# Optimization experiments

Measured on AMD Instinct MI355X. Metric: run time of the kernel, lower is better.

## Reference

```python
import jax, jax.numpy as jnp
import numpy as np

SR = 32000
N_FFT = 1024
HOP = 320
N_MELS = 128
PCEN_EPS = 1e-6
LN_EPS = 1e-6


def _hz_to_mel(f):
    return 2595.0 * np.log10(1.0 + f / 700.0)


def _mel_to_hz(m):
    return 700.0 * (10.0 ** (m / 2595.0) - 1.0)


def make_mel_fb():
    # HTK-scale triangular mel filterbank, [n_freqs, n_mels] (torchaudio default)
    n_freqs = N_FFT // 2 + 1
    mels = np.linspace(_hz_to_mel(0.0), _hz_to_mel(SR / 2.0), N_MELS + 2)
    f_pts = _mel_to_hz(mels)                       # [n_mels+2]
    all_freqs = np.linspace(0.0, SR / 2.0, n_freqs)
    f_diff = f_pts[1:] - f_pts[:-1]
    slopes = f_pts[None, :] - all_freqs[:, None]   # [n_freqs, n_mels+2]
    down = -slopes[:, :-2] / f_diff[:-1]
    up = slopes[:, 2:] / f_diff[1:]
    fb = np.maximum(0.0, np.minimum(down, up))
    return fb.astype(np.float32)


def setup_inputs() -> dict:
    key = jax.random.key(0)
    x = jax.random.normal(key, (16, 320000), dtype=jnp.float32)
    return {
        "x": x,
        "mel_fb": jnp.asarray(make_mel_fb()),
        "log_s": jnp.asarray(np.log(0.025), dtype=jnp.float32),
        "log_alpha": jnp.asarray(np.log(0.98), dtype=jnp.float32),
        "log_delta": jnp.asarray(np.log(2.0), dtype=jnp.float32),
        "log_r": jnp.asarray(np.log(0.5), dtype=jnp.float32),
    }


def reference(x, mel_fb, log_s, log_alpha, log_delta, log_r):
    B, T = x.shape
    pad = N_FFT // 2
    xp = jnp.pad(x, ((0, 0), (pad, pad)), mode="reflect")
    n_frames = 1 + (xp.shape[1] - N_FFT) // HOP           # = T//HOP + 1
    idx = jnp.arange(n_frames)[:, None] * HOP + jnp.arange(N_FFT)[None, :]
    frames = xp[:, idx]                                    # [B, F, N_FFT]
    # periodic Hann window (torch.hann_window default)
    win = 0.5 * (1.0 - jnp.cos(2.0 * jnp.pi * jnp.arange(N_FFT) / N_FFT))
    spec = jnp.fft.rfft(frames * win, axis=-1)             # [B, F, N_FFT//2+1]
    power = spec.real ** 2 + spec.imag ** 2                # power spectrogram
    E = jnp.einsum("bfk,km->bfm", power, mel_fb)           # [B, F, M] mel energies

    s = jnp.exp(log_s)
    alpha = jnp.exp(log_alpha)
    delta = jnp.exp(log_delta)
    r = jnp.exp(log_r)

    # Causal exponential smoother M(t) = (1-s) M(t-1) + s E(t), M init = first frame
    E_t = jnp.swapaxes(E, 0, 1)                            # [F, B, M]

    def step(m, e):
        m = (1.0 - s) * m + s * e
        return m, m

    _, M_t = jax.lax.scan(step, E_t[0], E_t)
    smooth = jnp.swapaxes(M_t, 0, 1)                       # [B, F, M]

    pcen = (E / (PCEN_EPS + smooth) ** alpha + delta) ** r - delta ** r

    # affine-free layer_norm over last dim (n_mels), eps=1e-6
    mu = jnp.mean(pcen, axis=-1, keepdims=True)
    var = jnp.var(pcen, axis=-1, keepdims=True)
    return (pcen - mu) / jnp.sqrt(var + LN_EPS)
```

## Files before the change

### kernel.cpp

```cpp
#include <hip/hip_runtime.h>
#include <math.h>

#define SRATE   32000
#define NFFT    1024
#define HOP     320
#define NBINS   513
#define NMELS   128
#define NFRAMES 1001
#define NB      16
#define TLEN    320000
#define PCEN_EPS 1e-6f
#define LN_EPS   1e-6f
#define MAXW     64

#define CL      16
#define NCHUNK  63

#define CPF     4
#define LPITCH  33

__device__ __constant__ static const int BR5_[1] = {0};
constexpr int BR5[32] = {0,16,8,24,4,20,12,28,2,18,10,26,6,22,14,30,
                         1,17,9,25,5,21,13,29,3,19,11,27,7,23,15,31};

__device__ __forceinline__ void fft32(float2* y) {
    constexpr float C16[16] = {
        1.f, 0.98078528f, 0.92387953f, 0.83146961f,
        0.70710678f, 0.55557023f, 0.38268343f, 0.19509032f,
        0.f, -0.19509032f, -0.38268343f, -0.55557023f,
        -0.70710678f, -0.83146961f, -0.92387953f, -0.98078528f};
    constexpr float S16[16] = {
        0.f, 0.19509032f, 0.38268343f, 0.55557023f,
        0.70710678f, 0.83146961f, 0.92387953f, 0.98078528f,
        1.f, 0.98078528f, 0.92387953f, 0.83146961f,
        0.70710678f, 0.55557023f, 0.38268343f, 0.19509032f};
    #pragma unroll
    for (int h = 16; h >= 1; h >>= 1) {
        #pragma unroll
        for (int b = 0; b < 32; b += 2 * h) {
            #pragma unroll
            for (int j = 0; j < h; ++j) {
                float2 u = y[b + j], w = y[b + j + h];
                float sr = u.x - w.x, si = u.y - w.y;
                y[b + j] = make_float2(u.x + w.x, u.y + w.y);
                const float wr = C16[j * (16 / h)];
                const float wi = -S16[j * (16 / h)];
                y[b + j + h] = make_float2(sr * wr - si * wi, sr * wi + si * wr);
            }
        }
    }
}

__global__ __launch_bounds__(256) void k_prep(
    const float* __restrict__ fb, int* __restrict__ kmin, int* __restrict__ klen,
    float* __restrict__ wv, float* __restrict__ winT, float2* __restrict__ twrow)
{
    const int blk = blockIdx.x;
    const int tid = threadIdx.x;
    if (blk < NMELS) {
        const int m = blk;
        __shared__ int smin[4], smax[4];
        int lmin = 1 << 30, lmax = -1;
        for (int k = tid; k < NBINS; k += 256) {
            if (fb[k * NMELS + m] > 0.f) {
                if (k < lmin) lmin = k;
                if (k > lmax) lmax = k;
            }
        }
        #pragma unroll
        for (int off = 32; off; off >>= 1) {
            int om = __shfl_xor(lmin, off); if (om < lmin) lmin = om;
            int ox = __shfl_xor(lmax, off); if (ox > lmax) lmax = ox;
        }
        if ((tid & 63) == 0) { smin[tid >> 6] = lmin; smax[tid >> 6] = lmax; }
        __syncthreads();
        int k0 = min(min(smin[0], smin[1]), min(smin[2], smin[3]));
        int k1 = max(max(smax[0], smax[1]), max(smax[2], smax[3]));
        int L  = (k1 < 0) ? 0 : min(k1 - k0 + 1, MAXW);
        if (tid == 0) { kmin[m] = (k1 < 0) ? 0 : k0; klen[m] = L; }
        if (tid < L) wv[m * MAXW + tid] = fb[(k0 + tid) * NMELS + m];
    } else {
        const int i = (blk - NMELS) * 256 + tid;
        if (i < NFFT) {
            float sp = sinpif((float)i * (1.0f / (float)NFFT));
            winT[((i & 31) << 5) | (i >> 5)] = sp * sp;
        } else {
            const int e = i - NFFT;
            const int c = e >> 5, k1 = e & 31;
            const int n = c * k1;
            float sn, cn;
            sincospif((float)n * (1.0f / 512.0f), &sn, &cn);
            twrow[e] = make_float2(cn, -sn);
        }
    }
}

__global__ __launch_bounds__(256) void k_melspec(
    const float* __restrict__ x,
    const int*   __restrict__ kmin,
    const int*   __restrict__ klen,
    const float* __restrict__ wv,
    const float* __restrict__ fb,
    const float* __restrict__ winT,
    const float2* __restrict__ twrow,
    float* __restrict__ E,
    int usePacked)
{
    __shared__ float2 Ld[CPF][LPITCH * 32];

    const int tid = threadIdx.x;
    const int g   = blockIdx.x;

    if (tid < 32 * CPF) {
        const int v = tid >> 5, c = tid & 31;
        const int fa = 8 * g + 2 * v, fbf = fa + 1;
        const int ba = fa / NFRAMES,  ta = fa  - ba * NFRAMES;
        const int bb = fbf / NFRAMES, tb = fbf - bb * NFRAMES;
        const float* xa = x + (size_t)ba * TLEN;
        const float* xb = x + (size_t)bb * TLEN;
        const int basea = ta * HOP - (NFFT / 2);
        const int baseb = tb * HOP - (NFFT / 2);
        float2 y[32];
        const bool safe = (basea >= 0) && (baseb >= 0) &&
                          (basea + NFFT - 1 < TLEN) && (baseb + NFFT - 1 < TLEN);
        if (usePacked && safe) {
            #pragma unroll
            for (int r = 0; r < 32; ++r) {
                const int i = c + 32 * r;
                const float w = winT[(c << 5) + r];
                y[r] = make_float2(xa[basea + i] * w, xb[baseb + i] * w);
            }
        } else {
            #pragma unroll
            for (int r = 0; r < 32; ++r) {
                const int i = c + 32 * r;
                int ja = basea + i;
                ja = (ja < 0) ? -ja : ((ja >= TLEN) ? (2 * TLEN - 2 - ja) : ja);
                int jb = baseb + i;
                jb = (jb < 0) ? -jb : ((jb >= TLEN) ? (2 * TLEN - 2 - jb) : jb);
                float w;
                if (usePacked) w = winT[(c << 5) + r];
                else { float sp = sinpif((float)i * (1.0f / (float)NFFT)); w = sp * sp; }
                y[r] = make_float2(xa[ja] * w, xb[jb] * w);
            }
        }
        fft32(y);
        const float2* trow = twrow + (c << 5);
        #pragma unroll
        for (int k1 = 0; k1 < 32; ++k1) {
            float2 val = y[BR5[k1]];
            float2 w;
            if (usePacked) w = trow[k1];
            else {
                float sn, cn;
                sincospif((float)(c * k1) * (1.0f / 512.0f), &sn, &cn);
                w = make_float2(cn, -sn);
            }
            Ld[v][LPITCH * c + k1] =
                make_float2(val.x * w.x - val.y * w.y,
                            val.x * w.y + val.y * w.x);
        }
    }
    __syncthreads();

    if (tid < 32 * CPF) {
        const int v = tid >> 5, k1 = tid & 31;
        float2 y[32];
        #pragma unroll
        for (int cc = 0; cc < 32; ++cc) y[cc] = Ld[v][LPITCH * cc + k1];
        fft32(y);
        #pragma unroll
        for (int k2 = 0; k2 < 32; ++k2)
            Ld[v][LPITCH * k2 + k1] = y[BR5[k2]];
    }
    __syncthreads();

    {
        const int m  = tid & 127;
        const int vh = tid >> 7;
        #pragma unroll
        for (int q = 0; q < 2; ++q) {
            const int vv = vh + 2 * q;
            const int f0 = 8 * g + 2 * vv;
            float acc0 = 0.f, acc1 = 0.f;
            if (usePacked) {
                const int k0 = kmin[m], L = klen[m];
                const float* w = wv + m * MAXW;
                for (int j = 0; j < L; ++j) {
                    const int k  = k0 + j;
                    const int kr = (NFFT - k) & (NFFT - 1);
                    float2 Z  = Ld[vv][LPITCH * (k  >> 5) + (k  & 31)];
                    float2 Zr = Ld[vv][LPITCH * (kr >> 5) + (kr & 31)];
                    float x1r = Z.x + Zr.x, x1i = Z.y - Zr.y;
                    float x2r = Z.y + Zr.y, x2i = Zr.x - Z.x;
                    float ww = w[j];
                    acc0 += (x1r * x1r + x1i * x1i) * ww;
                    acc1 += (x2r * x2r + x2i * x2i) * ww;
                }
            } else {
                for (int k = 0; k < NBINS; ++k) {
                    const int kr = (NFFT - k) & (NFFT - 1);
                    float2 Z  = Ld[vv][LPITCH * (k  >> 5) + (k  & 31)];
                    float2 Zr = Ld[vv][LPITCH * (kr >> 5) + (kr & 31)];
                    float x1r = Z.x + Zr.x, x1i = Z.y - Zr.y;
                    float x2r = Z.y + Zr.y, x2i = Zr.x - Z.x;
                    float ww = fb[k * NMELS + m];
                    acc0 += (x1r * x1r + x1i * x1i) * ww;
                    acc1 += (x2r * x2r + x2i * x2i) * ww;
                }
            }
            E[(size_t)f0 * NMELS + m]       = 0.25f * acc0;
            E[(size_t)(f0 + 1) * NMELS + m] = 0.25f * acc1;
        }
    }
}

__global__ __launch_bounds__(256) void k_pcen_chunk(
    const float* __restrict__ E, float* __restrict__ Bws,
    float* __restrict__ E0ws, const float* __restrict__ p_ls)
{
    const int gid = blockIdx.x * blockDim.x + threadIdx.x;
    const int m = gid & (NMELS - 1);
    const int c = (gid >> 7) % NCHUNK;
    const int b = gid / (NMELS * NCHUNK);

    const float s = expf(p_ls[0]);
    const float a = 1.f - s;

    const int t0 = c * CL;
    const int L  = (t0 + CL <= NFRAMES) ? CL : (NFRAMES - t0);
    const float* col = E + (size_t)b * NFRAMES * NMELS + m;

    if (c == 0) E0ws[b * NMELS + m] = col[0];

    float Bacc;
    if (L == CL) {
        float e[CL];
        #pragma unroll
        for (int j = 0; j < CL; ++j)
            e[j] = col[(size_t)(t0 + j) * NMELS];
        float p0 = 0.f, p1 = 0.f, p2 = 0.f, p3 = 0.f;
        #pragma unroll
        for (int u = 0; u < 4; ++u) {
            p0 = a * p0 + s * e[u];
            p1 = a * p1 + s * e[4 + u];
            p2 = a * p2 + s * e[8 + u];
            p3 = a * p3 + s * e[12 + u];
        }
        const float a2 = a * a, a4 = a2 * a2, a8 = a4 * a4, a12 = a8 * a4;
        Bacc = a12 * p0 + a8 * p1 + a4 * p2 + p3;
    } else {
        Bacc = 0.f;
        for (int j = 0; j < L; ++j)
            Bacc = a * Bacc + s * col[(size_t)(t0 + j) * NMELS];
    }
    Bws[gid] = Bacc;
}

__global__ __launch_bounds__(256) void k_pcen_ln(
    float* __restrict__ E, const float* __restrict__ Bws,
    const float* __restrict__ E0ws,
    const float* __restrict__ p_ls, const float* __restrict__ p_la,
    const float* __restrict__ p_ld, const float* __restrict__ p_lr)
{
    __shared__ float sm[2 * CL][NMELS];

    const int tid  = threadIdx.x;
    const int half = tid >> 7;
    const int m    = tid & 127;
    const int b    = blockIdx.x >> 5;
    const int cp   = blockIdx.x & 31;
    const int c    = cp * 2 + half;

    const float s     = expf(p_ls[0]);
    const float alpha = expf(p_la[0]);
    const float delta = expf(p_ld[0]);
    const float r     = expf(p_lr[0]);
    const float dr    = __powf(delta, r);
    const float a     = 1.f - s;
    const float a2 = a * a, a4 = a2 * a2, a8 = a4 * a4;
    const float a16 = a8 * a8;

    if (c < NCHUNK) {
        float M = E0ws[b * NMELS + m];
        const float* Bcol = Bws + (size_t)b * NCHUNK * NMELS + m;
        int cc = 0;
        for (; cc + 8 <= c; cc += 8) {
            float b0 = Bcol[(size_t)(cc + 0) * NMELS];
            float b1 = Bcol[(size_t)(cc + 1) * NMELS];
            float b2 = Bcol[(size_t)(cc + 2) * NMELS];
            float b3 = Bcol[(size_t)(cc + 3) * NMELS];
            float b4 = Bcol[(size_t)(cc + 4) * NMELS];
            float b5 = Bcol[(size_t)(cc + 5) * NMELS];
            float b6 = Bcol[(size_t)(cc + 6) * NMELS];
            float b7 = Bcol[(size_t)(cc + 7) * NMELS];
            M = a16 * M + b0; M = a16 * M + b1; M = a16 * M + b2; M = a16 * M + b3;
            M = a16 * M + b4; M = a16 * M + b5; M = a16 * M + b6; M = a16 * M + b7;
        }
        for (; cc < c; ++cc)
            M = a16 * M + Bcol[(size_t)cc * NMELS];

        const int t0 = c * CL;
        const int L  = (t0 + CL <= NFRAMES) ? CL : (NFRAMES - t0);
        const float* col = E + ((size_t)b * NFRAMES + t0) * NMELS + m;
        for (int j = 0; j < L; ++j) {
            float e = col[(size_t)j * NMELS];
            M = a * M + s * e;
            float den = __powf(PCEN_EPS + M, alpha);
            sm[half * CL + j][m] = __powf(e / den + delta, r) - dr;
        }
    }
    __syncthreads();

    const int wid  = tid >> 6;
    const int lane = tid & 63;
    for (int row = wid; row < 2 * CL; row += 4) {
        const int cc = cp * 2 + (row >> 4);
        if (cc >= NCHUNK) continue;
        const int j   = row & (CL - 1);
        const int tt0 = cc * CL;
        const int LL  = (tt0 + CL <= NFRAMES) ? CL : (NFRAMES - tt0);
        if (j >= LL) continue;
        float v0 = sm[row][lane], v1 = sm[row][lane + 64];
        float sum = v0 + v1;
        float sq  = v0 * v0 + v1 * v1;
        #pragma unroll
        for (int off = 32; off; off >>= 1) {
            sum += __shfl_xor(sum, off);
            sq  += __shfl_xor(sq,  off);
        }
        float mu  = sum * (1.f / 128.f);
        float var = sq * (1.f / 128.f) - mu * mu;
        float inv = rsqrtf(var + LN_EPS);
        float* p = E + ((size_t)b * NFRAMES + tt0 + j) * NMELS;
        p[lane]      = (v0 - mu) * inv;
        p[lane + 64] = (v1 - mu) * inv;
    }
}

__global__ __launch_bounds__(256) void k_pcen_serial(
    float* __restrict__ E,
    const float* __restrict__ p_ls, const float* __restrict__ p_la,
    const float* __restrict__ p_ld, const float* __restrict__ p_lr)
{
    const int gid = blockIdx.x * blockDim.x + threadIdx.x;
    const int b = gid >> 7;
    const int m = gid & 127;

    const float s     = expf(p_ls[0]);
    const float alpha = expf(p_la[0]);
    const float delta = expf(p_ld[0]);
    const float r     = expf(p_lr[0]);
    const float dr    = powf(delta, r);
    const float a     = 1.f - s;

    float* col = E + (size_t)b * NFRAMES * NMELS + m;
    float M = col[0];
    for (int t = 0; t < NFRAMES; ++t) {
        float e = col[(size_t)t * NMELS];
        M = a * M + s * e;
        float den = __powf(PCEN_EPS + M, alpha);
        float p   = __powf(e / den + delta, r) - dr;
        col[(size_t)t * NMELS] = p;
    }
}

__global__ __launch_bounds__(256) void k_ln(float* __restrict__ out) {
    const int wid  = threadIdx.x >> 6;
    const int lane = threadIdx.x & 63;
    const int row  = blockIdx.x * 4 + wid;
    float* p = out + (size_t)row * NMELS;
    float v0 = p[lane], v1 = p[lane + 64];
    float sum = v0 + v1;
    float sq  = v0 * v0 + v1 * v1;
    #pragma unroll
    for (int off = 32; off; off >>= 1) {
        sum += __shfl_xor(sum, off);
        sq  += __shfl_xor(sq,  off);
    }
    float mu  = sum * (1.f / 128.f);
    float var = sq * (1.f / 128.f) - mu * mu;
    float inv = rsqrtf(var + LN_EPS);
    p[lane]      = (v0 - mu) * inv;
    p[lane + 64] = (v1 - mu) * inv;
}

extern "C" void kernel_launch(void* const* d_in, const int* in_sizes, int n_in,
                              void* d_out, int out_size, void* d_ws, size_t ws_size,
                              hipStream_t stream) {
    const float* x   = (const float*)d_in[0];
    const float* fb  = (const float*)d_in[1];
    const float* lsp = (const float*)d_in[2];
    const float* lap = (const float*)d_in[3];
    const float* ldp = (const float*)d_in[4];
    const float* lrp = (const float*)d_in[5];
    float* out = (float*)d_out;

    const size_t packElems = 128 + 128 + 8192 + 1024 + 2048;
    const size_t scanElems = (size_t)NB * NCHUNK * NMELS;
    const size_t needPack  = packElems * 4;
    const size_t needScan  = (packElems + scanElems + (size_t)NB * NMELS) * 4;

    int usePacked = (ws_size >= needPack) ? 1 : 0;
    int useScan   = (ws_size >= needScan) ? 1 : 0;

    int*    kmin  = (int*)d_ws;
    int*    klen  = kmin + NMELS;
    float*  wv    = (float*)(klen + NMELS);
    float*  winT  = wv + (size_t)NMELS * MAXW;
    float2* twrow = (float2*)(winT + NFFT);
    float*  Bws   = (float*)(twrow + 1024);
    float*  E0ws  = Bws + scanElems;

    if (usePacked)
        k_prep<<<NMELS + 8, 256, 0, stream>>>(fb, kmin, klen, wv, winT, twrow);

    k_melspec<<<NB * NFRAMES / 8, 256, 0, stream>>>(
        x, kmin, klen, wv, fb, winT, twrow, out, usePacked);

    if (useScan) {
        const int nThread = NB * NCHUNK * NMELS;
        k_pcen_chunk<<<nThread / 256, 256, 0, stream>>>(out, Bws, E0ws, lsp);
        k_pcen_ln<<<NB * 32, 256, 0, stream>>>(out, Bws, E0ws, lsp, lap, ldp, lrp);
    } else {
        k_pcen_serial<<<(NB * NMELS) / 256, 256, 0, stream>>>(out, lsp, lap, ldp, lrp);
        k_ln<<<(NB * NFRAMES) / 4, 256, 0, stream>>>(out);
    }
}
```

Before: 93.94 us.

## Restructure melspec kernel: 64-thread blocks, vectorized frame staging, XOR-swizzled LDS

The mel-spectrogram kernel now uses 64-thread blocks processing 4 frames (one wavefront, no idle lanes) instead of 256-thread blocks where only half the threads did FFT work. Frame samples are loaded with coalesced float4 reads and windowed into shared memory, then transposed into registers, replacing strided per-thread scalar global loads. The padded LDS layout is replaced by an XOR swizzle to avoid bank conflicts without padding. This adds an extra shared-memory staging pass and barriers, and doubles the block count.

```diff
diff --git a/kernel.cpp b/kernel.cpp
--- a/kernel.cpp
+++ b/kernel.cpp
@@ -16,12 +16,10 @@
 #define CL      16
 #define NCHUNK  63
 
-#define CPF     4
-#define LPITCH  33
-
-__device__ __constant__ static const int BR5_[1] = {0};
 constexpr int BR5[32] = {0,16,8,24,4,20,12,28,2,18,10,26,6,22,14,30,
                          1,17,9,25,5,21,13,29,3,19,11,27,7,23,15,31};
+
+__device__ __forceinline__ int SL(int r, int c) { return (r << 5) | (c ^ r); }
 
 __device__ __forceinline__ void fft32(float2* y) {
     constexpr float C16[16] = {
@@ -53,7 +51,7 @@
 
 __global__ __launch_bounds__(256) void k_prep(
     const float* __restrict__ fb, int* __restrict__ kmin, int* __restrict__ klen,
-    float* __restrict__ wv, float* __restrict__ winT, float2* __restrict__ twrow)
+    float* __restrict__ wv, float* __restrict__ win, float2* __restrict__ twrow)
 {
     const int blk = blockIdx.x;
     const int tid = threadIdx.x;
@@ -83,7 +81,7 @@
         const int i = (blk - NMELS) * 256 + tid;
         if (i < NFFT) {
             float sp = sinpif((float)i * (1.0f / (float)NFFT));
-            winT[((i & 31) << 5) | (i >> 5)] = sp * sp;
+            win[i] = sp * sp;
         } else {
             const int e = i - NFFT;
             const int c = e >> 5, k1 = e & 31;
@@ -95,56 +93,71 @@
     }
 }
 
-__global__ __launch_bounds__(256) void k_melspec(
+__global__ __launch_bounds__(64) void k_melspec(
     const float* __restrict__ x,
     const int*   __restrict__ kmin,
     const int*   __restrict__ klen,
     const float* __restrict__ wv,
     const float* __restrict__ fb,
-    const float* __restrict__ winT,
+    const float* __restrict__ win_g,
     const float2* __restrict__ twrow,
     float* __restrict__ E,
     int usePacked)
 {
-    __shared__ float2 Ld[CPF][LPITCH * 32];
+    __shared__ float2 Ld[2][1024];
 
     const int tid = threadIdx.x;
     const int g   = blockIdx.x;
-
-    if (tid < 32 * CPF) {
-        const int v = tid >> 5, c = tid & 31;
-        const int fa = 8 * g + 2 * v, fbf = fa + 1;
-        const int ba = fa / NFRAMES,  ta = fa  - ba * NFRAMES;
-        const int bb = fbf / NFRAMES, tb = fbf - bb * NFRAMES;
-        const float* xa = x + (size_t)ba * TLEN;
-        const float* xb = x + (size_t)bb * TLEN;
-        const int basea = ta * HOP - (NFFT / 2);
-        const int baseb = tb * HOP - (NFFT / 2);
-        float2 y[32];
-        const bool safe = (basea >= 0) && (baseb >= 0) &&
-                          (basea + NFFT - 1 < TLEN) && (baseb + NFFT - 1 < TLEN);
-        if (usePacked && safe) {
-            #pragma unroll
-            for (int r = 0; r < 32; ++r) {
-                const int i = c + 32 * r;
-                const float w = winT[(c << 5) + r];
-                y[r] = make_float2(xa[basea + i] * w, xb[baseb + i] * w);
-            }
-        } else {
-            #pragma unroll
-            for (int r = 0; r < 32; ++r) {
-                const int i = c + 32 * r;
-                int ja = basea + i;
-                ja = (ja < 0) ? -ja : ((ja >= TLEN) ? (2 * TLEN - 2 - ja) : ja);
-                int jb = baseb + i;
-                jb = (jb < 0) ? -jb : ((jb >= TLEN) ? (2 * TLEN - 2 - jb) : jb);
-                float w;
-                if (usePacked) w = winT[(c << 5) + r];
-                else { float sp = sinpif((float)i * (1.0f / (float)NFFT)); w = sp * sp; }
-                y[r] = make_float2(xa[ja] * w, xb[jb] * w);
-            }
-        }
-        fft32(y);
+    const int v   = tid >> 5;
+    const int c   = tid & 31;
+
+    float2* T  = Ld[v];
+    float*  fS = (float*)T;
+
+    const int fa  = 4 * g + 2 * v, fbf = fa + 1;
+    const int ba  = fa / NFRAMES,  ta  = fa  - ba * NFRAMES;
+    const int bb  = fbf / NFRAMES, tb  = fbf - bb * NFRAMES;
+    const float* xa = x + (size_t)ba * TLEN;
+    const float* xb = x + (size_t)bb * TLEN;
+    const int basea = ta * HOP - (NFFT / 2);
+    const int baseb = tb * HOP - (NFFT / 2);
+    const bool safe = basea >= 0 && baseb >= 0 &&
+                      (basea + NFFT <= TLEN) && (baseb + NFFT <= TLEN);
+
+    if (usePacked && safe) {
+        const float4* xa4 = (const float4*)(xa + basea);
+        const float4* xb4 = (const float4*)(xb + baseb);
+        const float4* w4  = (const float4*)win_g;
+        float4* S4 = (float4*)fS;
+        #pragma unroll
+        for (int q = 0; q < 8; ++q) {
+            float4 a = xa4[q * 32 + c], b = xb4[q * 32 + c], w = w4[q * 32 + c];
+            S4[q * 32 + c]       = make_float4(a.x * w.x, a.y * w.y, a.z * w.z, a.w * w.w);
+            S4[256 + q * 32 + c] = make_float4(b.x * w.x, b.y * w.y, b.z * w.z, b.w * w.w);
+        }
+    } else {
+        for (int i = c; i < NFFT; i += 32) {
+            int ja = basea + i;
+            ja = (ja < 0) ? -ja : ((ja >= TLEN) ? (2 * TLEN - 2 - ja) : ja);
+            int jb = baseb + i;
+            jb = (jb < 0) ? -jb : ((jb >= TLEN) ? (2 * TLEN - 2 - jb) : jb);
+            float w;
+            if (usePacked) w = win_g[i];
+            else { float sp = sinpif((float)i * (1.0f / (float)NFFT)); w = sp * sp; }
+            fS[i]        = xa[ja] * w;
+            fS[NFFT + i] = xb[jb] * w;
+        }
+    }
+    __syncthreads();
+
+    float2 y[32];
+    #pragma unroll
+    for (int r = 0; r < 32; ++r)
+        y[r] = make_float2(fS[c + 32 * r], fS[NFFT + c + 32 * r]);
+    __syncthreads();
+
+    fft32(y);
+    {
         const float2* trow = twrow + (c << 5);
         #pragma unroll
         for (int k1 = 0; k1 < 32; ++k1) {
@@ -156,32 +169,25 @@
                 sincospif((float)(c * k1) * (1.0f / 512.0f), &sn, &cn);
                 w = make_float2(cn, -sn);
             }
-            Ld[v][LPITCH * c + k1] =
-                make_float2(val.x * w.x - val.y * w.y,
-                            val.x * w.y + val.y * w.x);
+            T[SL(c, k1)] = make_float2(val.x * w.x - val.y * w.y,
+                                       val.x * w.y + val.y * w.x);
         }
     }
     __syncthreads();
 
-    if (tid < 32 * CPF) {
-        const int v = tid >> 5, k1 = tid & 31;
-        float2 y[32];
-        #pragma unroll
-        for (int cc = 0; cc < 32; ++cc) y[cc] = Ld[v][LPITCH * cc + k1];
-        fft32(y);
-        #pragma unroll
-        for (int k2 = 0; k2 < 32; ++k2)
-            Ld[v][LPITCH * k2 + k1] = y[BR5[k2]];
-    }
+    #pragma unroll
+    for (int cc = 0; cc < 32; ++cc) y[cc] = T[SL(cc, c)];
+    fft32(y);
+    #pragma unroll
+    for (int k2 = 0; k2 < 32; ++k2) T[SL(k2, c)] = y[BR5[k2]];
     __syncthreads();
 
-    {
-        const int m  = tid & 127;
-        const int vh = tid >> 7;
-        #pragma unroll
-        for (int q = 0; q < 2; ++q) {
-            const int vv = vh + 2 * q;
-            const int f0 = 8 * g + 2 * vv;
+    for (int vv = 0; vv < 2; ++vv) {
+        const float2* Tv = Ld[vv];
+        const int f0 = 4 * g + 2 * vv;
+        #pragma unroll
+        for (int h = 0; h < 2; ++h) {
+            const int m = tid + 64 * h;
             float acc0 = 0.f, acc1 = 0.f;
             if (usePacked) {
                 const int k0 = kmin[m], L = klen[m];
@@ -189,8 +195,8 @@
                 for (int j = 0; j < L; ++j) {
                     const int k  = k0 + j;
                     const int kr = (NFFT - k) & (NFFT - 1);
-                    float2 Z  = Ld[vv][LPITCH * (k  >> 5) + (k  & 31)];
-                    float2 Zr = Ld[vv][LPITCH * (kr >> 5) + (kr & 31)];
+                    float2 Z  = Tv[SL(k >> 5,  k & 31)];
+                    float2 Zr = Tv[SL(kr >> 5, kr & 31)];
                     float x1r = Z.x + Zr.x, x1i = Z.y - Zr.y;
                     float x2r = Z.y + Zr.y, x2i = Zr.x - Z.x;
                     float ww = w[j];
@@ -200,8 +206,8 @@
             } else {
                 for (int k = 0; k < NBINS; ++k) {
                     const int kr = (NFFT - k) & (NFFT - 1);
-                    float2 Z  = Ld[vv][LPITCH * (k  >> 5) + (k  & 31)];
-                    float2 Zr = Ld[vv][LPITCH * (kr >> 5) + (kr & 31)];
+                    float2 Z  = Tv[SL(k >> 5,  k & 31)];
+                    float2 Zr = Tv[SL(kr >> 5, kr & 31)];
                     float x1r = Z.x + Zr.x, x1i = Z.y - Zr.y;
                     float x2r = Z.y + Zr.y, x2i = Zr.x - Z.x;
                     float ww = fb[k * NMELS + m];
@@ -407,16 +413,16 @@
     int*    kmin  = (int*)d_ws;
     int*    klen  = kmin + NMELS;
     float*  wv    = (float*)(klen + NMELS);
-    float*  winT  = wv + (size_t)NMELS * MAXW;
-    float2* twrow = (float2*)(winT + NFFT);
+    float*  win   = wv + (size_t)NMELS * MAXW;
+    float2* twrow = (float2*)(win + NFFT);
     float*  Bws   = (float*)(twrow + 1024);
     float*  E0ws  = Bws + scanElems;
 
     if (usePacked)
-        k_prep<<<NMELS + 8, 256, 0, stream>>>(fb, kmin, klen, wv, winT, twrow);
-
-    k_melspec<<<NB * NFRAMES / 8, 256, 0, stream>>>(
-        x, kmin, klen, wv, fb, winT, twrow, out, usePacked);
+        k_prep<<<NMELS + 8, 256, 0, stream>>>(fb, kmin, klen, wv, win, twrow);
+
+    k_melspec<<<NB * NFRAMES / 4, 64, 0, stream>>>(
+        x, kmin, klen, wv, fb, win, twrow, out, usePacked);
 
     if (useScan) {
         const int nThread = NB * NCHUNK * NMELS;
```

Measured after the change: 94.80 us. Within noise of the previous version (+0.9%).
